# Optimization experiments

Measured on AMD Instinct MI355X. Metric: run time of the kernel, lower is better.

## Reference

```python
import jax, jax.numpy as jnp
import numpy as np

GAMMA = 1.0
BIG = 1e8  # boundary value used by the original numba kernel


def setup_inputs() -> dict:
    key = jax.random.key(0)
    k1, k2 = jax.random.split(key)
    N, M, d = 4096, 4096, 64
    x = jax.random.normal(k1, (N, d), dtype=jnp.float32)
    y = jax.random.normal(k2, (M, d), dtype=jnp.float32)
    return {"x": x, "y": y}


def _soft_dtw(D, gamma):
    """Soft-DTW DP R[N,M] via anti-diagonal wavefront scan.

    Matches compute_softdtw: R padded with BIG, R[0,0]=0,
    R[i,j] = D[i-1,j-1] + softmin_gamma(R[i-1,j-1], R[i-1,j], R[i,j-1]).
    Diagonals are stored as length-(N+2) vectors indexed by i (j = k - i).
    """
    N, M = D.shape
    ii = jnp.arange(1, N + 1)          # cell row indices 1..N
    inf = jnp.full((N + 2,), BIG, D.dtype)
    r_km2 = inf.at[0].set(0.0)          # diagonal k=0: only R[0,0]=0
    r_km1 = inf                         # diagonal k=1: all boundary

    def step(carry, k):
        r_km2, r_km1 = carry
        j = k - ii                      # column index per row on this diagonal
        valid = (j >= 1) & (j <= M)
        r0 = -r_km2[ii - 1] / gamma     # R[i-1, j-1]
        r1 = -r_km1[ii - 1] / gamma     # R[i-1, j]
        r2 = -r_km1[ii] / gamma         # R[i,   j-1]
        rmax = jnp.maximum(jnp.maximum(r0, r1), r2)
        rsum = jnp.exp(r0 - rmax) + jnp.exp(r1 - rmax) + jnp.exp(r2 - rmax)
        softmin = -gamma * (jnp.log(rsum) + rmax)
        jc = jnp.clip(j - 1, 0, M - 1)
        d_diag = D[ii - 1, jc]          # D[i-1, j-1] along this diagonal
        val = jnp.where(valid, d_diag + softmin, BIG)
        r_k = inf.at[1:N + 1].set(val)
        return (r_km1, r_k), None

    ks = jnp.arange(2, N + M + 1)
    (_, r_last), _ = jax.lax.scan(step, (r_km2, r_km1), ks)
    return r_last[N]                    # R[N, M]


def reference(x, y):
    # squared-euclidean distance matrix: sum((x_i - y_j)^2)
    x2 = jnp.sum(x * x, axis=1)
    y2 = jnp.sum(y * y, axis=1)
    D = x2[:, None] + y2[None, :] - 2.0 * (x @ y.T)  # [N, M]
    N, M = D.shape
    r = _soft_dtw(D, GAMMA)
    return r / (N + M)                   # open_end=False path
```

## Files before the change

kernel.cpp:

```cpp
#include <hip/hip_runtime.h>
#include <hip/hip_fp16.h>

#define Nn 4096
#define Mm 4096
#define NB 64
#define CH 16
#define NCHUNK 260
#define NCHUNKP 262
#define HPITCH 4352
#define HOFF 64
#define LOG2E 1.4426950408889634f
#define LN2 0.6931471805599453f
#define BIGX (1 << 23)
#define CUSH 5

typedef unsigned long long ull;

__device__ __forceinline__ float hw_exp2(float x) { return __builtin_amdgcn_exp2f(x); }
__device__ __forceinline__ float hw_log2(float x) { return __builtin_amdgcn_logf(x); }

__device__ __forceinline__ float dpp_shl1(float v) {
    int r = __builtin_amdgcn_update_dpp(0, __float_as_int(v), 0x130, 0xF, 0xF, false);
    return __int_as_float(r);
}
__device__ __forceinline__ int dpp_shl1_i(int v) {
    return __builtin_amdgcn_update_dpp(0, v, 0x130, 0xF, 0xF, false);
}
__device__ __forceinline__ ull packmx(float m, int X) {
    return (ull)__float_as_uint(m) | ((ull)(unsigned)X << 32);
}

__device__ __forceinline__ int packcell(float dv) {
    float nf = __builtin_rintf(dv);
    int NI = (int)nf;
    if (NI > 2047) NI = 2047;
    if (NI < -2048) NI = -2048;
    float KM = hw_exp2(nf - dv);
    unsigned kb = __float_as_uint(KM);
    unsigned low20 = (kb - 0x3F000000u) >> 4;
    return (NI << 20) | (int)low20;
}

#define UPK(KM, NI, S) \
    int NI = (S) >> 20; \
    float KM = __uint_as_float(0x3F000000u + (((unsigned)(S) & 0xFFFFFu) << 4));

#define GLOAD4(dst, ptr) \
    asm volatile("global_load_dwordx4 %0, %1, off" : "=v"(dst) : "v"(ptr))
#define GLOADH(dst, ptr) \
    asm volatile("global_load_dwordx2 %0, %1, off sc1" : "=v"(dst) : "v"(ptr))
#define GSTOREH(ptr, val) \
    asm volatile("global_store_dwordx2 %0, %1, off sc1" :: "v"(ptr), "v"(val))
#define WAITV(n) do { \
    asm volatile("s_waitcnt vmcnt(" #n ")" ::: "memory"); \
    __builtin_amdgcn_sched_barrier(0); } while (0)

__global__ __launch_bounds__(256) void dist_kernel(const float* __restrict__ x,
                                                   const float* __restrict__ y,
                                                   int* __restrict__ DskI) {
    __shared__ float xs[64][65];
    __shared__ float ys[80][65];
    __shared__ float dt[64][81];
    __shared__ float x2s[64], y2s[80];
    const int b = blockIdx.y, tj = blockIdx.x, tid = threadIdx.x;

    const float4* x4 = (const float4*)(x + (size_t)b * 64 * 64);
#pragma unroll
    for (int i = 0; i < 4; ++i) {
        int idx = tid + i * 256;
        int r = idx >> 4, c = (idx & 15) * 4;
        float4 v = x4[idx];
        xs[r][c] = v.x; xs[r][c + 1] = v.y; xs[r][c + 2] = v.z; xs[r][c + 3] = v.w;
    }
#pragma unroll
    for (int i = 0; i < 5; ++i) {
        int idx = tid + i * 256;
        int r = idx >> 4, c = (idx & 15) * 4;
        int rowg = tj * 64 + r; if (rowg > Mm - 1) rowg = Mm - 1;
        float4 w = ((const float4*)(y + (size_t)rowg * 64))[c >> 2];
        ys[r][c] = w.x; ys[r][c + 1] = w.y; ys[r][c + 2] = w.z; ys[r][c + 3] = w.w;
    }
    __syncthreads();

    if (tid < 64) {
        float a = 0.f;
#pragma unroll 8
        for (int k = 0; k < 64; ++k) a += xs[tid][k] * xs[tid][k];
        x2s[tid] = a;
    } else if (tid < 144) {
        int r = tid - 64;
        float a = 0.f;
#pragma unroll 8
        for (int k = 0; k < 64; ++k) a += ys[r][k] * ys[r][k];
        y2s[r] = a;
    }
    __syncthreads();

    const int r0 = (tid >> 4) * 4, c0 = (tid & 15) * 5;
    float acc[4][5] = {{0.f}};
#pragma unroll 4
    for (int k = 0; k < 64; ++k) {
        float a0 = xs[r0][k], a1 = xs[r0 + 1][k], a2 = xs[r0 + 2][k], a3 = xs[r0 + 3][k];
#pragma unroll
        for (int j = 0; j < 5; ++j) {
            float bj = ys[c0 + j][k];
            acc[0][j] = fmaf(a0, bj, acc[0][j]);
            acc[1][j] = fmaf(a1, bj, acc[1][j]);
            acc[2][j] = fmaf(a2, bj, acc[2][j]);
            acc[3][j] = fmaf(a3, bj, acc[3][j]);
        }
    }
#pragma unroll
    for (int i = 0; i < 4; ++i)
#pragma unroll
        for (int j = 0; j < 5; ++j)
            dt[r0 + i][c0 + j] =
                (x2s[r0 + i] + y2s[c0 + j] - 2.0f * acc[i][j]) * LOG2E;
    __syncthreads();

    const int l = tid & 63, q = tid >> 6;
    const int ci = ((l + 15) >> 4) + q;
    const int jj0 = 16 * ci - l;
    int S[16];
#pragma unroll
    for (int t = 0; t < 16; ++t) S[t] = packcell(dt[l][jj0 + t]);
    {
        int* dst = DskI + (((size_t)b * NCHUNKP + 4 * tj + ci) * 64 + l) * 16;
        int4* d4 = (int4*)dst;
        d4[0] = make_int4(S[0],  S[1],  S[2],  S[3]);
        d4[1] = make_int4(S[4],  S[5],  S[6],  S[7]);
        d4[2] = make_int4(S[8],  S[9],  S[10], S[11]);
        d4[3] = make_int4(S[12], S[13], S[14], S[15]);
    }
    if (tj == 0 && q == 0) {
        const int cif = l >> 4;
        int Sf[16];
#pragma unroll
        for (int t = 0; t < 16; ++t) {
            int j = 16 * cif - l + t; if (j < 0) j = 0;
            Sf[t] = packcell(dt[l][j]);
        }
        int* dst = DskI + (((size_t)b * NCHUNKP + cif) * 64 + l) * 16;
        int4* d4 = (int4*)dst;
        d4[0] = make_int4(Sf[0],  Sf[1],  Sf[2],  Sf[3]);
        d4[1] = make_int4(Sf[4],  Sf[5],  Sf[6],  Sf[7]);
        d4[2] = make_int4(Sf[8],  Sf[9],  Sf[10], Sf[11]);
        d4[3] = make_int4(Sf[12], Sf[13], Sf[14], Sf[15]);
    }
}

#define STEP(KM, NI, IDX) do {                                                \
    float upM = __int_as_float(__builtin_amdgcn_update_dpp(                   \
        __float_as_int(hRotM), __float_as_int(lM), 0x138, 0xF, 0xF, false));  \
    int   upX = __builtin_amdgcn_update_dpp(hRotX, lX, 0x138, 0xF, 0xF, false); \
    float dgM = psM; int dgX = psX;                                           \
    hRotM = dpp_shl1(hRotM); hRotX = dpp_shl1_i(hRotX);                       \
    int Xm = min(min(dgX, upX), lX);                                          \
    float ssum = ldexpf(dgM, Xm - dgX) + ldexpf(upM, Xm - upX) +              \
                 ldexpf(lM, Xm - lX);                                         \
    psM = upM; psX = upX;                                                     \
    lM = ssum * (KM);                                                         \
    lX = Xm + (NI);                                                           \
    sm##IDX = lM; sx##IDX = lX;                                               \
} while (0)

#define LATCH(IDX) do {                                                       \
    unsigned rm_ = (unsigned)__builtin_amdgcn_readlane(                       \
        __float_as_int(sm##IDX), 63);                                         \
    unsigned rx_ = (unsigned)__builtin_amdgcn_readlane(sx##IDX, 63);          \
    if (l == 48 + (IDX)) { svM = rm_; svX = rx_; }                            \
} while (0)

#define BODY(DA, DB, DC, DD, HB) do {                                          \
    WAITV(7);                                                                  \
    hRotM = __uint_as_float((unsigned)(HB));                                   \
    hRotX = (int)(unsigned)((HB) >> 32);                                       \
    if (!doH) { hRotM = 0.5f; hRotX = BIGX; }                                  \
    {   int hc_ = c + 2; if (hc_ > 255) hc_ = 255;   \
        const ull* hp_ = HinB + 16 * hc_ + 1 + lt;                             \
        GLOADH(HB, hp_); }                                                     \
    if (doH && (c <= 255)) {       \
        while (__ballot(!(hRotM > 0.f))) {           \
            __builtin_amdgcn_s_sleep(16);                                      \
            ull v_ = __hip_atomic_load(&HinB[16 * c + 1 + lt],                 \
                                       __ATOMIC_RELAXED, __HIP_MEMORY_SCOPE_AGENT); \
            hRotM = __uint_as_float((unsigned)v_);                             \
            hRotX = (int)(unsigned)(v_ >> 32);                                 \
        }                                                                      \
    }                                                                          \
    UPK(k0,  n0,  (DA).x); STEP(k0,  n0,  0);                                  \
    UPK(k1,  n1,  (DA).y); STEP(k1,  n1,  1);                                  \
    UPK(k2,  n2,  (DA).z); STEP(k2,  n2,  2);                                  \
    UPK(k3,  n3,  (DA).w); STEP(k3,  n3,  3);                                  \
    UPK(k4,  n4,  (DB).x); STEP(k4,  n4,  4);                                  \
    UPK(k5,  n5,  (DB).y); STEP(k5,  n5,  5);                                  \
    UPK(k6,  n6,  (DB).z); STEP(k6,  n6,  6);                                  \
    UPK(k7,  n7,  (DB).w); STEP(k7,  n7,  7);                                  \
    UPK(k8,  n8,  (DC).x); STEP(k8,  n8,  8);                                  \
    UPK(k9,  n9,  (DC).y); STEP(k9,  n9,  9);                                  \
    UPK(k10, n10, (DC).z); STEP(k10, n10, 10);                                 \
    UPK(k11, n11, (DC).w); STEP(k11, n11, 11);                                 \
    UPK(k12, n12, (DD).x); STEP(k12, n12, 12);                                 \
    UPK(k13, n13, (DD).y); STEP(k13, n13, 13);                                 \
    UPK(k14, n14, (DD).z); STEP(k14, n14, 14);                                 \
    if (c == NCHUNK - 1) { rTM = lM; rTX = lX; }         \
    UPK(k15, n15, (DD).w); STEP(k15, n15, 15);                                 \
    LATCH(0);  LATCH(1);  LATCH(2);  LATCH(3);                                 \
    LATCH(4);  LATCH(5);  LATCH(6);  LATCH(7);                                 \
    LATCH(8);  LATCH(9);  LATCH(10); LATCH(11);                                \
    LATCH(12); LATCH(13); LATCH(14); LATCH(15);                                \
    {             \
        unsigned mb_ = __float_as_uint(lM);                                    \
        lX += (int)((mb_ >> 23) & 0xFFu) - 126;                                \
        lM = __uint_as_float((mb_ & 0x807FFFFFu) | 0x3F000000u); }             \
    {   const int4* pD_ = (const int4*)(Db + (size_t)(c + 2) * 1024);          \
        GLOAD4(DA, pD_); GLOAD4(DB, pD_ + 1);                                  \
        GLOAD4(DC, pD_ + 2); GLOAD4(DD, pD_ + 3); }                            \
    if (l >= 48) {         \
        ull* sp_ = HoutB + 16 * c - 62 + (l - 48);                             \
        ull sv_ = (ull)svM | ((ull)svX << 32);                                 \
        GSTOREH(sp_, sv_); }                                                   \
    ++c;                                                                       \
} while (0)

__global__ __launch_bounds__(64, 1) void dp_kernel(const int* __restrict__ DskI,
                                                   ull* __restrict__ H,
                                                   float* __restrict__ out) {
    const int l = threadIdx.x;
    const int b = blockIdx.x;
    const bool lastBand = (b == NB - 1);
    const bool isL63 = (l == 63);
    const int lt = l & 15;
    const int* __restrict__ Db = DskI + ((size_t)b * NCHUNKP * 64 + l) * 16;
    const ull* __restrict__ HinB = H + (size_t)b * HPITCH + HOFF;
    ull* __restrict__ HoutB = H + (size_t)(b + 1) * HPITCH + HOFF;
    const bool doH = (b > 0);

    float lM = 0.5f;  int lX = BIGX;
    float psM = 0.5f; int psX = (b == 0 && l == 0) ? -1 : BIGX;
    float hRotM; int hRotX;
    ull hb0, hb1;
    int4 dA0, dB0, dC0, dD0, dA1, dB1, dC1, dD1;
    float rTM = 0.5f; int rTX = 0;
    unsigned svM = 0, svX = 0;
    float sm0, sm1, sm2, sm3, sm4, sm5, sm6, sm7;
    float sm8, sm9, sm10, sm11, sm12, sm13, sm14, sm15;
    int sx0, sx1, sx2, sx3, sx4, sx5, sx6, sx7;
    int sx8, sx9, sx10, sx11, sx12, sx13, sx14, sx15;

    if (doH) {
        const int gs = 16 * (CUSH - 1) + 1 + lt;
        while (1) {
            ull v = __hip_atomic_load(&HinB[gs], __ATOMIC_RELAXED,
                                      __HIP_MEMORY_SCOPE_AGENT);
            if (!__ballot(!(__uint_as_float((unsigned)v) > 0.f))) break;
            __builtin_amdgcn_s_sleep(8);
        }
    }

    {
        const int4* p = (const int4*)Db;
        GLOAD4(dA0, p);     GLOAD4(dB0, p + 1);
        GLOAD4(dC0, p + 2); GLOAD4(dD0, p + 3);
        const int4* q = (const int4*)(Db + 1024);
        GLOAD4(dA1, q);     GLOAD4(dB1, q + 1);
        GLOAD4(dC1, q + 2); GLOAD4(dD1, q + 3);
    }
    if (doH) {
        GLOADH(hb0, HinB + 1 + lt);
        GLOADH(hb1, HinB + CH + 1 + lt);
    } else {
        hb0 = packmx(0.5f, BIGX);
        hb1 = hb0;
    }
    asm volatile("s_waitcnt vmcnt(0)" ::: "memory");
    __builtin_amdgcn_sched_barrier(0);

    int c = 0;
    for (int it = 0; it < NCHUNK / 2; ++it) {
        BODY(dA0, dB0, dC0, dD0, hb0);
        BODY(dA1, dB1, dC1, dD1, hb1);
    }

    if (lastBand && isL63) {
        float rpr = (float)rTX - hw_log2(rTM);
        out[0] = rpr * (LN2 / (float)(Nn + Mm));
    }
}

extern "C" void kernel_launch(void* const* d_in, const int* in_sizes, int n_in,
                              void* d_out, int out_size, void* d_ws, size_t ws_size,
                              hipStream_t stream) {
    const float* x = (const float*)d_in[0];
    const float* y = (const float*)d_in[1];
    float* out = (float*)d_out;

    char* ws = (char*)d_ws;
    int* DskI = (int*)ws;
    size_t dskBytes = (size_t)NB * NCHUNKP * 64 * 16 * sizeof(int);
    ull* H = (ull*)(ws + dskBytes);

    dist_kernel<<<dim3(64, 64), 256, 0, stream>>>(x, y, DskI);
    dp_kernel<<<NB, 64, 0, stream>>>(DskI, H, out);
}
```

Baseline: 1.085 ms.

## Broadcast halo values via readlane scalars instead of DPP rotate chain

The incoming halo row from the previous band is now broadcast into 16 scalar registers with readlane per chunk. The update DPP then uses these uniform values, so the per-step DPP shift-left rotation of hRotM/hRotX is gone. Halo prefetch drops from two chunks ahead to one, using a single hb buffer, and the startup cushion falls from 5 to 4 chunks. This shortens the per-step dependency chain and the inter-band lag, but the halo load now has less time to land, so the spin-wait may hit more often.

```diff
diff --git a/kernel.cpp b/kernel.cpp
--- a/kernel.cpp
+++ b/kernel.cpp
@@ -12,20 +12,13 @@
 #define LOG2E 1.4426950408889634f
 #define LN2 0.6931471805599453f
 #define BIGX (1 << 23)
-#define CUSH 5
+#define CUSH 4
 
 typedef unsigned long long ull;
 
 __device__ __forceinline__ float hw_exp2(float x) { return __builtin_amdgcn_exp2f(x); }
 __device__ __forceinline__ float hw_log2(float x) { return __builtin_amdgcn_logf(x); }
 
-__device__ __forceinline__ float dpp_shl1(float v) {
-    int r = __builtin_amdgcn_update_dpp(0, __float_as_int(v), 0x130, 0xF, 0xF, false);
-    return __int_as_float(r);
-}
-__device__ __forceinline__ int dpp_shl1_i(int v) {
-    return __builtin_amdgcn_update_dpp(0, v, 0x130, 0xF, 0xF, false);
-}
 __device__ __forceinline__ ull packmx(float m, int X) {
     return (ull)__float_as_uint(m) | ((ull)(unsigned)X << 32);
 }
@@ -149,12 +142,16 @@
     }
 }
 
+#define RL(IDX) \
+    unsigned hm##IDX = (unsigned)__builtin_amdgcn_readlane((int)hbLo, IDX); \
+    unsigned hx##IDX = (unsigned)__builtin_amdgcn_readlane((int)hbHi, IDX);
+
 #define STEP(KM, NI, IDX) do {                                                \
+    int vIm_ = (int)hm##IDX; int vIx_ = (int)hx##IDX;                         \
     float upM = __int_as_float(__builtin_amdgcn_update_dpp(                   \
-        __float_as_int(hRotM), __float_as_int(lM), 0x138, 0xF, 0xF, false));  \
-    int   upX = __builtin_amdgcn_update_dpp(hRotX, lX, 0x138, 0xF, 0xF, false); \
+        vIm_, __float_as_int(lM), 0x138, 0xF, 0xF, false));                   \
+    int   upX = __builtin_amdgcn_update_dpp(vIx_, lX, 0x138, 0xF, 0xF, false); \
     float dgM = psM; int dgX = psX;                                           \
-    hRotM = dpp_shl1(hRotM); hRotX = dpp_shl1_i(hRotX);                       \
     int Xm = min(min(dgX, upX), lX);                                          \
     float ssum = ldexpf(dgM, Xm - dgX) + ldexpf(upM, Xm - upX) +              \
                  ldexpf(lM, Xm - lX);                                         \
@@ -171,23 +168,27 @@
     if (l == 48 + (IDX)) { svM = rm_; svX = rx_; }                            \
 } while (0)
 
-#define BODY(DA, DB, DC, DD, HB) do {                                          \
-    WAITV(7);                                                                  \
-    hRotM = __uint_as_float((unsigned)(HB));                                   \
-    hRotX = (int)(unsigned)((HB) >> 32);                                       \
-    if (!doH) { hRotM = 0.5f; hRotX = BIGX; }                                  \
-    {   int hc_ = c + 2; if (hc_ > 255) hc_ = 255;   \
-        const ull* hp_ = HinB + 16 * hc_ + 1 + lt;                             \
-        GLOADH(HB, hp_); }                                                     \
-    if (doH && (c <= 255)) {       \
-        while (__ballot(!(hRotM > 0.f))) {           \
+#define BODY(DA, DB, DC, DD) do {                                              \
+    WAITV(5);                                                                  \
+    if (doH && (c <= 255)) {        \
+        while (__ballot(!(__uint_as_float((unsigned)hb) > 0.f))) {             \
             __builtin_amdgcn_s_sleep(16);                                      \
-            ull v_ = __hip_atomic_load(&HinB[16 * c + 1 + lt],                 \
-                                       __ATOMIC_RELAXED, __HIP_MEMORY_SCOPE_AGENT); \
-            hRotM = __uint_as_float((unsigned)v_);                             \
-            hRotX = (int)(unsigned)(v_ >> 32);                                 \
+            hb = __hip_atomic_load(&HinB[16 * c + 1 + lt],                     \
+                                   __ATOMIC_RELAXED, __HIP_MEMORY_SCOPE_AGENT);\
         }                                                                      \
     }                                                                          \
+    unsigned hbLo = (unsigned)hb, hbHi = (unsigned)(hb >> 32);                 \
+    RL(0)  RL(1)  RL(2)  RL(3)  RL(4)  RL(5)  RL(6)  RL(7)                     \
+    RL(8)  RL(9)  RL(10) RL(11) RL(12) RL(13) RL(14) RL(15)                    \
+    if (!doH) {                                                                \
+        hm0 = hm1 = hm2 = hm3 = hm4 = hm5 = hm6 = hm7 = 0x3F000000u;           \
+        hm8 = hm9 = hm10 = hm11 = hm12 = hm13 = hm14 = hm15 = 0x3F000000u;     \
+        hx0 = hx1 = hx2 = hx3 = hx4 = hx5 = hx6 = hx7 = (unsigned)BIGX;        \
+        hx8 = hx9 = hx10 = hx11 = hx12 = hx13 = hx14 = hx15 = (unsigned)BIGX;  \
+    }                                                                          \
+    {   int hc_ = c + 1; if (hc_ > 255) hc_ = 255;   \
+        const ull* hp_ = HinB + 16 * hc_ + 1 + lt;                             \
+        GLOADH(hb, hp_); }                                                     \
     UPK(k0,  n0,  (DA).x); STEP(k0,  n0,  0);                                  \
     UPK(k1,  n1,  (DA).y); STEP(k1,  n1,  1);                                  \
     UPK(k2,  n2,  (DA).z); STEP(k2,  n2,  2);                                  \
@@ -205,6 +206,14 @@
     UPK(k14, n14, (DD).z); STEP(k14, n14, 14);                                 \
     if (c == NCHUNK - 1) { rTM = lM; rTX = lX; }         \
     UPK(k15, n15, (DD).w); STEP(k15, n15, 15);                                 \
+    asm volatile("" : "+v"(sm0), "+v"(sm1), "+v"(sm2),  "+v"(sm3),             \
+                      "+v"(sm4), "+v"(sm5), "+v"(sm6),  "+v"(sm7),             \
+                      "+v"(sm8), "+v"(sm9), "+v"(sm10), "+v"(sm11),            \
+                      "+v"(sm12), "+v"(sm13), "+v"(sm14), "+v"(sm15));         \
+    asm volatile("" : "+v"(sx0), "+v"(sx1), "+v"(sx2),  "+v"(sx3),             \
+                      "+v"(sx4), "+v"(sx5), "+v"(sx6),  "+v"(sx7),             \
+                      "+v"(sx8), "+v"(sx9), "+v"(sx10), "+v"(sx11),            \
+                      "+v"(sx12), "+v"(sx13), "+v"(sx14), "+v"(sx15));         \
     LATCH(0);  LATCH(1);  LATCH(2);  LATCH(3);                                 \
     LATCH(4);  LATCH(5);  LATCH(6);  LATCH(7);                                 \
     LATCH(8);  LATCH(9);  LATCH(10); LATCH(11);                                \
@@ -238,8 +247,7 @@
 
     float lM = 0.5f;  int lX = BIGX;
     float psM = 0.5f; int psX = (b == 0 && l == 0) ? -1 : BIGX;
-    float hRotM; int hRotX;
-    ull hb0, hb1;
+    ull hb;
     int4 dA0, dB0, dC0, dD0, dA1, dB1, dC1, dD1;
     float rTM = 0.5f; int rTX = 0;
     unsigned svM = 0, svX = 0;
@@ -266,20 +274,15 @@
         GLOAD4(dA1, q);     GLOAD4(dB1, q + 1);
         GLOAD4(dC1, q + 2); GLOAD4(dD1, q + 3);
     }
-    if (doH) {
-        GLOADH(hb0, HinB + 1 + lt);
-        GLOADH(hb1, HinB + CH + 1 + lt);
-    } else {
-        hb0 = packmx(0.5f, BIGX);
-        hb1 = hb0;
-    }
+    GLOADH(hb, HinB + 1 + lt);
     asm volatile("s_waitcnt vmcnt(0)" ::: "memory");
     __builtin_amdgcn_sched_barrier(0);
+    if (!doH) hb = packmx(0.5f, BIGX);
 
     int c = 0;
     for (int it = 0; it < NCHUNK / 2; ++it) {
-        BODY(dA0, dB0, dC0, dD0, hb0);
-        BODY(dA1, dB1, dC1, dD1, hb1);
+        BODY(dA0, dB0, dC0, dD0);
+        BODY(dA1, dB1, dC1, dD1);
     }
 
     if (lastBand && isL63) {
```

New measurement: 1.025 ms. 5.5% less time.
